# Kernel optimization log

Hardware: AMD Instinct MI355X
Metric: run time of the kernel (lower is better)

Reference implementation:

```python
import jax, jax.numpy as jnp
import numpy as np
from jax import lax

T, B, INP, HS, OUT = 256, 128, 1024, 1024, 1024


def setup_inputs() -> dict:
    key = jax.random.key(0)
    ks = jax.random.split(key, 7)
    s = 1.0 / np.sqrt(HS)  # scale params to keep tanh out of deep saturation
    return {
        "data": jax.random.normal(ks[0], (T, B, INP), jnp.float32),
        "W_ih": jax.random.normal(ks[1], (INP, HS), jnp.float32) * s,
        "W_hh": jax.random.normal(ks[2], (HS, HS), jnp.float32) * s,
        "b_i": jax.random.normal(ks[3], (HS,), jnp.float32) * s,
        "b_h": jax.random.normal(ks[4], (HS,), jnp.float32) * s,
        "W_out": jax.random.normal(ks[5], (OUT, HS), jnp.float32) * s,
        "b_out": jax.random.normal(ks[6], (OUT,), jnp.float32) * s,
    }


def reference(data, W_ih, W_hh, b_i, b_h, W_out, b_out):
    # Elman RNN: h_{t+1} = tanh(x_t @ W_ih + b_i + h_t @ W_hh + b_h)
    bias = b_i + b_h
    h0 = jnp.zeros((data.shape[1], W_hh.shape[0]), data.dtype)

    def step(h, x_t):
        h_new = jnp.tanh(x_t @ W_ih + h @ W_hh + bias)
        return h_new, None

    h_final, _ = lax.scan(step, h0, data)
    # nn.Linear: out = h @ W_out.T + b_out
    return h_final @ W_out.T + b_out
```

## Files before the change

kernel.cpp:

```cpp
#include <hip/hip_runtime.h>
#include <hip/hip_bf16.h>
#include <math.h>


typedef __attribute__((ext_vector_type(8))) short bf16x8;
typedef __attribute__((ext_vector_type(4))) float f32x4;
typedef __attribute__((ext_vector_type(4))) unsigned short u16x4;
typedef __attribute__((ext_vector_type(4))) unsigned int u32x4;
typedef __attribute__((ext_vector_type(2))) unsigned int u32x2;

#define TT 256
#define BB 128
#define HS 1024
#define H_ELEMS (BB * HS)

__device__ __forceinline__ short f2bf(float x) {
  __hip_bfloat16 b = __float2bfloat16(x);
  return *reinterpret_cast<short*>(&b);
}
__device__ __forceinline__ float bf2f(unsigned short s) {
  unsigned int u = ((unsigned int)s) << 16;
  float f;
  __builtin_memcpy(&f, &u, 4);
  return f;
}
__device__ __forceinline__ float fast_exp2(float x) {
#if __has_builtin(__builtin_amdgcn_exp2f)
  return __builtin_amdgcn_exp2f(x);
#else
  return exp2f(x);
#endif
}
__device__ __forceinline__ float fast_rcp(float x) {
#if __has_builtin(__builtin_amdgcn_rcpf)
  return __builtin_amdgcn_rcpf(x);
#else
  return 1.0f / x;
#endif
}
__device__ __forceinline__ float fast_tanh(float x) {
  float xc = fminf(fmaxf(x, -9.0f), 9.0f);
  float e = fast_exp2(2.8853900817779268f * xc);
  return (e - 1.0f) * fast_rcp(e + 1.0f);
}

__device__ __forceinline__ void mall_load_b128(u32x4* dst, const void* p) {
  asm volatile("global_load_dwordx4 %0, %1, off sc0 sc1" : "=v"(*dst) : "v"(p) : "memory");
}
__device__ __forceinline__ void mall_store_b64(void* p, u32x2 v) {
  asm volatile("global_store_dwordx2 %0, %1, off sc0 sc1" :: "v"(p), "v"(v) : "memory");
}
__device__ __forceinline__ void mall_store_b32(void* p, unsigned v) {
  asm volatile("global_store_dword %0, %1, off sc0 sc1" :: "v"(p), "v"(v) : "memory");
}
__device__ __forceinline__ unsigned mall_poll_b32(const void* p) {
  unsigned v;
  asm volatile("global_load_dword %0, %1, off sc0 sc1" : "=v"(v) : "v"(p) : "memory");
  asm volatile("s_waitcnt vmcnt(0)" : "+v"(v));
  return v;
}
__device__ __forceinline__ void wait_vm0() {
  asm volatile("s_waitcnt vmcnt(0)" ::: "memory");
}
#define TIE16(d)                                                        \
  asm volatile("s_waitcnt vmcnt(0)"                                     \
               : "+v"(d[0]), "+v"(d[1]), "+v"(d[2]), "+v"(d[3]),        \
                 "+v"(d[4]), "+v"(d[5]), "+v"(d[6]), "+v"(d[7]),        \
                 "+v"(d[8]), "+v"(d[9]), "+v"(d[10]), "+v"(d[11]),      \
                 "+v"(d[12]), "+v"(d[13]), "+v"(d[14]), "+v"(d[15]))

__global__ __launch_bounds__(256) void cvt_data(const float* __restrict__ src,
                                                __hip_bfloat16* __restrict__ dst) {
  size_t i = ((size_t)blockIdx.x * 256 + threadIdx.x) * 8;
  f32x4 a = *reinterpret_cast<const f32x4*>(src + i);
  f32x4 b = *reinterpret_cast<const f32x4*>(src + i + 4);
  bf16x8 v;
  v[0] = f2bf(a[0]); v[1] = f2bf(a[1]); v[2] = f2bf(a[2]); v[3] = f2bf(a[3]);
  v[4] = f2bf(b[0]); v[5] = f2bf(b[1]); v[6] = f2bf(b[2]); v[7] = f2bf(b[3]);
  *reinterpret_cast<bf16x8*>(dst + i) = v;
}

__global__ __launch_bounds__(256) void cvt_tr(const float* __restrict__ src,
                                              __hip_bfloat16* __restrict__ dst) {
  __shared__ __hip_bfloat16 T[64][72];
  const int tid = threadIdx.x;
  const int k0 = blockIdx.y * 64, n0 = blockIdx.x * 64;
  const int r = tid >> 4, c4 = (tid & 15) * 4;
#pragma unroll
  for (int p = 0; p < 4; ++p) {
    int kk = r + p * 16;
    f32x4 v = *reinterpret_cast<const f32x4*>(src + (size_t)(k0 + kk) * 1024 + n0 + c4);
#pragma unroll
    for (int j = 0; j < 4; ++j) T[c4 + j][kk] = __float2bfloat16(v[j]);
  }
  __syncthreads();
  const int rr = tid >> 3, u = tid & 7;
#pragma unroll
  for (int p = 0; p < 2; ++p) {
    int R = rr + p * 32;
    *reinterpret_cast<bf16x8*>(dst + (size_t)(n0 + R) * 1024 + k0 + u * 8) =
        *reinterpret_cast<const bf16x8*>(&T[R][u * 8]);
  }
}

template <bool ABF>
__global__ __launch_bounds__(256) void gemm_xw2(
    const void* __restrict__ Ain,
    const __hip_bfloat16* __restrict__ Bt,
    const float* __restrict__ b_i,
    const float* __restrict__ b_h,
    __hip_bfloat16* __restrict__ P) {
  __shared__ __hip_bfloat16 As[128][72];
  __shared__ __hip_bfloat16 Bs[128][72];

  const int tid = threadIdx.x;
  const int m0 = blockIdx.y * 128, n0 = blockIdx.x * 128;
  const int wave = tid >> 6, lane = tid & 63;
  const int wm = wave & 1, wn = wave >> 1;
  const int quad = lane >> 4, l16 = lane & 15;
  const int sr = tid >> 3, su = tid & 7;

  f32x4 acc[4][4] = {};

  for (int k0 = 0; k0 < 1024; k0 += 64) {
    __syncthreads();
#pragma unroll
    for (int p = 0; p < 4; ++p) {
      int row = sr + p * 32;
      bf16x8 av;
      if (ABF) {
        av = *reinterpret_cast<const bf16x8*>(
            (const __hip_bfloat16*)Ain + (size_t)(m0 + row) * 1024 + k0 + su * 8);
      } else {
        const float* ap = (const float*)Ain + (size_t)(m0 + row) * 1024 + k0 + su * 8;
        f32x4 x = *reinterpret_cast<const f32x4*>(ap);
        f32x4 y = *reinterpret_cast<const f32x4*>(ap + 4);
        av[0] = f2bf(x[0]); av[1] = f2bf(x[1]); av[2] = f2bf(x[2]); av[3] = f2bf(x[3]);
        av[4] = f2bf(y[0]); av[5] = f2bf(y[1]); av[6] = f2bf(y[2]); av[7] = f2bf(y[3]);
      }
      *reinterpret_cast<bf16x8*>(&As[row][su * 8]) = av;
      bf16x8 bv = *reinterpret_cast<const bf16x8*>(
          Bt + (size_t)(n0 + row) * 1024 + k0 + su * 8);
      *reinterpret_cast<bf16x8*>(&Bs[row][su * 8]) = bv;
    }
    __syncthreads();
#pragma unroll
    for (int kk = 0; kk < 2; ++kk) {
      bf16x8 af[4], bfr[4];
#pragma unroll
      for (int mi = 0; mi < 4; ++mi)
        af[mi] = *reinterpret_cast<const bf16x8*>(&As[wm * 64 + mi * 16 + l16][kk * 32 + quad * 8]);
#pragma unroll
      for (int ni = 0; ni < 4; ++ni)
        bfr[ni] = *reinterpret_cast<const bf16x8*>(&Bs[wn * 64 + ni * 16 + l16][kk * 32 + quad * 8]);
#pragma unroll
      for (int mi = 0; mi < 4; ++mi)
#pragma unroll
        for (int ni = 0; ni < 4; ++ni)
          acc[mi][ni] = __builtin_amdgcn_mfma_f32_16x16x32_bf16(af[mi], bfr[ni], acc[mi][ni], 0, 0, 0);
    }
  }

  float bias[4];
#pragma unroll
  for (int ni = 0; ni < 4; ++ni) {
    int col = n0 + wn * 64 + ni * 16 + l16;
    bias[ni] = b_i[col] + b_h[col];
  }
#pragma unroll
  for (int mi = 0; mi < 4; ++mi)
#pragma unroll
    for (int ni = 0; ni < 4; ++ni) {
      int row = m0 + wm * 64 + mi * 16 + quad * 4;
      int col = n0 + wn * 64 + ni * 16 + l16;
#pragma unroll
      for (int r = 0; r < 4; ++r)
        P[(size_t)(row + r) * 1024 + col] = __float2bfloat16(acc[mi][ni][r] + bias[ni]);
    }
}

__global__ __launch_bounds__(128) void rnn_scan5(
    const __hip_bfloat16* __restrict__ P,
    const float* __restrict__ W_hh,
    __hip_bfloat16* __restrict__ hbuf,
    unsigned* __restrict__ flags) {
  __shared__ __hip_bfloat16 Wt[32 * 1024];
  __shared__ __hip_bfloat16 Ht[16 * 1024];
  __shared__ __hip_bfloat16 Cs[16 * 36];

  const int tid = threadIdx.x;
  const int m = blockIdx.x & 7;
  const int ng = blockIdx.x >> 3;
  const int m0 = m * 16, n0 = ng * 32;

  for (int i = tid; i < 32 * 1024 / 4; i += 128) {
    int nq = i & 7, k = i >> 3;
    f32x4 v = *reinterpret_cast<const f32x4*>(W_hh + (size_t)k * 1024 + n0 + nq * 4);
#pragma unroll
    for (int j = 0; j < 4; ++j) {
      int nl = nq * 4 + j;
      int sg = (k >> 3) ^ (nl & 7);
      Wt[nl * 1024 + sg * 8 + (k & 7)] = __float2bfloat16(v[j]);
    }
  }
  __syncthreads();

  const int r8 = tid >> 3, s8 = tid & 7;
  const int w = tid >> 6, lane = tid & 63;
  const int quad = lane >> 4, l16 = lane & 15;
  const int nl = w * 16 + l16;
  const int col = n0 + nl;
  const int xorl = l16 & 7;
  const int crow = tid >> 3, cseg = tid & 7;
  unsigned* gflags = flags + m * 32;

  for (int t = 0; t < TT; ++t) {
    const __hip_bfloat16* hc = hbuf + (size_t)(t & 1) * H_ELEMS;
    __hip_bfloat16* hn = hbuf + (size_t)((t + 1) & 1) * H_ELEMS;

    const __hip_bfloat16* Pt =
        P + (size_t)t * H_ELEMS + (size_t)(m0 + quad * 4) * 1024 + col;
    unsigned short pv[4];
#pragma unroll
    for (int r = 0; r < 4; ++r)
      pv[r] = *reinterpret_cast<const unsigned short*>(Pt + (size_t)r * 1024);

    if (t > 0) {
      if (tid < 32) {
        const unsigned* fp = gflags + tid;
        int g = 0;
        while (mall_poll_b32(fp) < (unsigned)t && ++g < (1 << 18)) {}
      }
      __syncthreads();
    }

    {
      const char* src = (const char*)(hc + (size_t)(m0 + r8) * 1024) + s8 * 16;
      u32x4 d[16];
#pragma unroll
      for (int i = 0; i < 16; ++i) mall_load_b128(&d[i], src + i * 128);
      TIE16(d);
#pragma unroll
      for (int i = 0; i < 16; ++i) {
        int u = s8 + i * 8;
        int gp = u ^ (r8 & 7) ^ (u >> 4);
        *reinterpret_cast<u32x4*>(&Ht[r8 * 1024 + gp * 8]) = d[i];
      }
    }
    __syncthreads();

    f32x4 acc[4] = {{0.f, 0.f, 0.f, 0.f}, {0.f, 0.f, 0.f, 0.f},
                    {0.f, 0.f, 0.f, 0.f}, {0.f, 0.f, 0.f, 0.f}};
#pragma unroll
    for (int c = 0; c < 8; ++c) {
#pragma unroll
      for (int j = 0; j < 4; ++j) {
        int G = c * 16 + j * 4 + quad;
        int gp = G ^ xorl ^ c;
        bf16x8 af = *reinterpret_cast<const bf16x8*>(&Ht[l16 * 1024 + gp * 8]);
        int sg = G ^ (nl & 7);
        bf16x8 bfrag = *reinterpret_cast<const bf16x8*>(&Wt[nl * 1024 + sg * 8]);
        acc[j] = __builtin_amdgcn_mfma_f32_16x16x32_bf16(af, bfrag, acc[j], 0, 0, 0);
      }
    }

#pragma unroll
    for (int r = 0; r < 4; ++r) {
      float s = (acc[0][r] + acc[1][r]) + (acc[2][r] + acc[3][r]) + bf2f(pv[r]);
      Cs[(quad * 4 + r) * 36 + nl] = __float2bfloat16(fast_tanh(s));
    }
    __syncthreads();
    {
      u32x2 val = *reinterpret_cast<const u32x2*>(&Cs[crow * 36 + cseg * 4]);
      mall_store_b64(hn + (size_t)(m0 + crow) * 1024 + n0 + cseg * 4, val);
      wait_vm0();
    }
    __syncthreads();

    if (t != TT - 1 && tid == 0)
      mall_store_b32(gflags + ng, (unsigned)(t + 1));
  }
}

__global__ __launch_bounds__(256) void gemm_out(
    const __hip_bfloat16* __restrict__ h,
    const float* __restrict__ W_out,
    const float* __restrict__ b_out,
    float* __restrict__ out) {
  const int tid = threadIdx.x;
  const int wave = tid >> 6, lane = tid & 63;
  const int quad = lane >> 4, l16 = lane & 15;
  const int o = blockIdx.x * 64 + wave * 16 + l16;

  f32x4 acc[8] = {};
  for (int k0 = 0; k0 < 1024; k0 += 32) {
    f32x4 w0 = *reinterpret_cast<const f32x4*>(W_out + (size_t)o * 1024 + k0 + quad * 8);
    f32x4 w1 = *reinterpret_cast<const f32x4*>(W_out + (size_t)o * 1024 + k0 + quad * 8 + 4);
    bf16x8 bfr;
    bfr[0] = f2bf(w0[0]); bfr[1] = f2bf(w0[1]); bfr[2] = f2bf(w0[2]); bfr[3] = f2bf(w0[3]);
    bfr[4] = f2bf(w1[0]); bfr[5] = f2bf(w1[1]); bfr[6] = f2bf(w1[2]); bfr[7] = f2bf(w1[3]);
#pragma unroll
    for (int mi = 0; mi < 8; ++mi) {
      bf16x8 af = *reinterpret_cast<const bf16x8*>(h + (size_t)(mi * 16 + l16) * 1024 + k0 + quad * 8);
      acc[mi] = __builtin_amdgcn_mfma_f32_16x16x32_bf16(af, bfr, acc[mi], 0, 0, 0);
    }
  }
  const float bias = b_out[o];
#pragma unroll
  for (int mi = 0; mi < 8; ++mi)
#pragma unroll
    for (int r = 0; r < 4; ++r)
      out[(size_t)(mi * 16 + quad * 4 + r) * 1024 + o] = acc[mi][r] + bias;
}

extern "C" void kernel_launch(void* const* d_in, const int* in_sizes, int n_in,
                              void* d_out, int out_size, void* d_ws, size_t ws_size,
                              hipStream_t stream) {
  const float* data  = (const float*)d_in[0];
  const float* W_ih  = (const float*)d_in[1];
  const float* W_hh  = (const float*)d_in[2];
  const float* b_i   = (const float*)d_in[3];
  const float* b_h   = (const float*)d_in[4];
  const float* W_out = (const float*)d_in[5];
  const float* b_out = (const float*)d_in[6];
  float* out = (float*)d_out;

  char* ws = (char*)d_ws;
  const size_t OFF_P   = 0;
  const size_t OFF_H   = (size_t)TT * H_ELEMS * 2;
  const size_t OFF_FLG = OFF_H + 2 * H_ELEMS * 2;
  const size_t OFF_WT  = OFF_FLG + 1024;
  const size_t OFF_DB  = OFF_WT + 2u * 1024 * 1024;
  const size_t NEED_DB = OFF_DB + (size_t)TT * H_ELEMS * 2;

  __hip_bfloat16* P     = (__hip_bfloat16*)(ws + OFF_P);
  __hip_bfloat16* hbuf  = (__hip_bfloat16*)(ws + OFF_H);
  unsigned* flags       = (unsigned*)(ws + OFF_FLG);
  __hip_bfloat16* W_ihT = (__hip_bfloat16*)(ws + OFF_WT);
  __hip_bfloat16* dataB = (__hip_bfloat16*)(ws + OFF_DB);

  hipMemsetAsync(ws + OFF_H, 0, 2 * H_ELEMS * 2 + 1024, stream);

  cvt_tr<<<dim3(16, 16), 256, 0, stream>>>(W_ih, W_ihT);
  if (ws_size >= NEED_DB) {
    cvt_data<<<16384, 256, 0, stream>>>(data, dataB);
    gemm_xw2<true><<<dim3(8, 256), 256, 0, stream>>>(dataB, W_ihT, b_i, b_h, P);
  } else {
    gemm_xw2<false><<<dim3(8, 256), 256, 0, stream>>>(data, W_ihT, b_i, b_h, P);
  }
  rnn_scan5<<<256, 128, 0, stream>>>(P, W_hh, hbuf, flags);
  gemm_out<<<16, 256, 0, stream>>>(hbuf, W_out, b_out, out);
}
```

Before: 1.129 ms.

## Fuse input projection GEMM into recurrent scan kernel with per-timestep readiness counters

Merges the input-projection GEMM and the recurrent scan into one launch. The first 256 blocks run the scan and the extra 4096 blocks compute P tiles, each bumping a per-timestep counter, so the scan can start while later projection tiles are still being produced. The separate bf16 conversion pass over the input data is dropped in favour of converting inside the GEMM. The scan now loads h fragments straight from global memory into registers with staged waits instead of staging them through shared memory. The scan blocks spin on the counters, which relies on them being co-resident with the GEMM blocks and adds polling traffic.

Measured after the change: 1.429 ms. 1.27x slower.

```diff
diff --git a/kernel.cpp b/kernel.cpp
--- a/kernel.cpp
+++ b/kernel.cpp
@@ -5,7 +5,6 @@
 
 typedef __attribute__((ext_vector_type(8))) short bf16x8;
 typedef __attribute__((ext_vector_type(4))) float f32x4;
-typedef __attribute__((ext_vector_type(4))) unsigned short u16x4;
 typedef __attribute__((ext_vector_type(4))) unsigned int u32x4;
 typedef __attribute__((ext_vector_type(2))) unsigned int u32x2;
 
@@ -13,6 +12,7 @@
 #define BB 128
 #define HS 1024
 #define H_ELEMS (BB * HS)
+#define SMEM_BYTES 66688
 
 __device__ __forceinline__ short f2bf(float x) {
   __hip_bfloat16 b = __float2bfloat16(x);
@@ -44,8 +44,14 @@
   return (e - 1.0f) * fast_rcp(e + 1.0f);
 }
 
-__device__ __forceinline__ void mall_load_b128(u32x4* dst, const void* p) {
+__device__ __forceinline__ void mall_load_bf8(bf16x8* dst, const void* p) {
   asm volatile("global_load_dwordx4 %0, %1, off sc0 sc1" : "=v"(*dst) : "v"(p) : "memory");
+}
+__device__ __forceinline__ void mall_load_u16(unsigned* dst, const void* p) {
+  asm volatile("global_load_ushort %0, %1, off sc0 sc1" : "=v"(*dst) : "v"(p) : "memory");
+}
+__device__ __forceinline__ void mall_store_b128(void* p, u32x4 v) {
+  asm volatile("global_store_dwordx4 %0, %1, off sc0 sc1" :: "v"(p), "v"(v) : "memory");
 }
 __device__ __forceinline__ void mall_store_b64(void* p, u32x2 v) {
   asm volatile("global_store_dwordx2 %0, %1, off sc0 sc1" :: "v"(p), "v"(v) : "memory");
@@ -62,22 +68,14 @@
 __device__ __forceinline__ void wait_vm0() {
   asm volatile("s_waitcnt vmcnt(0)" ::: "memory");
 }
-#define TIE16(d)                                                        \
-  asm volatile("s_waitcnt vmcnt(0)"                                     \
-               : "+v"(d[0]), "+v"(d[1]), "+v"(d[2]), "+v"(d[3]),        \
-                 "+v"(d[4]), "+v"(d[5]), "+v"(d[6]), "+v"(d[7]),        \
-                 "+v"(d[8]), "+v"(d[9]), "+v"(d[10]), "+v"(d[11]),      \
-                 "+v"(d[12]), "+v"(d[13]), "+v"(d[14]), "+v"(d[15]))
-
-__global__ __launch_bounds__(256) void cvt_data(const float* __restrict__ src,
-                                                __hip_bfloat16* __restrict__ dst) {
-  size_t i = ((size_t)blockIdx.x * 256 + threadIdx.x) * 8;
-  f32x4 a = *reinterpret_cast<const f32x4*>(src + i);
-  f32x4 b = *reinterpret_cast<const f32x4*>(src + i + 4);
-  bf16x8 v;
-  v[0] = f2bf(a[0]); v[1] = f2bf(a[1]); v[2] = f2bf(a[2]); v[3] = f2bf(a[3]);
-  v[4] = f2bf(b[0]); v[5] = f2bf(b[1]); v[6] = f2bf(b[2]); v[7] = f2bf(b[3]);
-  *reinterpret_cast<bf16x8*>(dst + i) = v;
+#define WAITV(N) asm volatile("s_waitcnt vmcnt(" #N ")" ::: "memory")
+__device__ __forceinline__ void tie8(bf16x8& a, bf16x8& b, bf16x8& c, bf16x8& d,
+                                     bf16x8& e, bf16x8& f, bf16x8& g, bf16x8& h) {
+  asm volatile("" : "+v"(a), "+v"(b), "+v"(c), "+v"(d),
+                    "+v"(e), "+v"(f), "+v"(g), "+v"(h));
+}
+__device__ __forceinline__ void tie4u(unsigned& a, unsigned& b, unsigned& c, unsigned& d) {
+  asm volatile("" : "+v"(a), "+v"(b), "+v"(c), "+v"(d));
 }
 
 __global__ __launch_bounds__(256) void cvt_tr(const float* __restrict__ src,
@@ -103,92 +101,99 @@
   }
 }
 
-template <bool ABF>
-__global__ __launch_bounds__(256) void gemm_xw2(
-    const void* __restrict__ Ain,
-    const __hip_bfloat16* __restrict__ Bt,
+__global__ __launch_bounds__(128) void fused(
+    const float* __restrict__ data,
+    const __hip_bfloat16* __restrict__ W_ihT,
+    const float* __restrict__ W_hh,
     const float* __restrict__ b_i,
     const float* __restrict__ b_h,
-    __hip_bfloat16* __restrict__ P) {
-  __shared__ __hip_bfloat16 As[128][72];
-  __shared__ __hip_bfloat16 Bs[128][72];
-
+    __hip_bfloat16* __restrict__ P,
+    __hip_bfloat16* __restrict__ hbuf,
+    unsigned* __restrict__ flags,
+    unsigned* __restrict__ pcnt) {
+  __shared__ __attribute__((aligned(16))) unsigned char smem[SMEM_BYTES];
   const int tid = threadIdx.x;
-  const int m0 = blockIdx.y * 128, n0 = blockIdx.x * 128;
-  const int wave = tid >> 6, lane = tid & 63;
-  const int wm = wave & 1, wn = wave >> 1;
+  const int w = tid >> 6, lane = tid & 63;
   const int quad = lane >> 4, l16 = lane & 15;
-  const int sr = tid >> 3, su = tid & 7;
-
-  f32x4 acc[4][4] = {};
-
-  for (int k0 = 0; k0 < 1024; k0 += 64) {
-    __syncthreads();
-#pragma unroll
-    for (int p = 0; p < 4; ++p) {
-      int row = sr + p * 32;
-      bf16x8 av;
-      if (ABF) {
-        av = *reinterpret_cast<const bf16x8*>(
-            (const __hip_bfloat16*)Ain + (size_t)(m0 + row) * 1024 + k0 + su * 8);
-      } else {
-        const float* ap = (const float*)Ain + (size_t)(m0 + row) * 1024 + k0 + su * 8;
+
+  if (blockIdx.x >= 256) {
+    auto As = (__hip_bfloat16(*)[72])(smem);
+    auto Bs = (__hip_bfloat16(*)[72])(smem + 18432);
+    const int j = (int)blockIdx.x - 256;
+    const int mt = j >> 4, nt = j & 15;
+    const int m0g = mt * 128, n0g = nt * 64;
+    const int sr = tid >> 3, su = tid & 7;
+
+    float bias[4];
+#pragma unroll
+    for (int ni = 0; ni < 4; ++ni) {
+      int c = n0g + ni * 16 + l16;
+      bias[ni] = b_i[c] + b_h[c];
+    }
+
+    f32x4 acc[4][4] = {};
+    for (int k0 = 0; k0 < 1024; k0 += 64) {
+      __syncthreads();
+#pragma unroll
+      for (int p = 0; p < 8; ++p) {
+        int row = sr + p * 16;
+        const float* ap = data + (size_t)(m0g + row) * 1024 + k0 + su * 8;
         f32x4 x = *reinterpret_cast<const f32x4*>(ap);
         f32x4 y = *reinterpret_cast<const f32x4*>(ap + 4);
+        bf16x8 av;
         av[0] = f2bf(x[0]); av[1] = f2bf(x[1]); av[2] = f2bf(x[2]); av[3] = f2bf(x[3]);
         av[4] = f2bf(y[0]); av[5] = f2bf(y[1]); av[6] = f2bf(y[2]); av[7] = f2bf(y[3]);
-      }
-      *reinterpret_cast<bf16x8*>(&As[row][su * 8]) = av;
-      bf16x8 bv = *reinterpret_cast<const bf16x8*>(
-          Bt + (size_t)(n0 + row) * 1024 + k0 + su * 8);
-      *reinterpret_cast<bf16x8*>(&Bs[row][su * 8]) = bv;
-    }
-    __syncthreads();
-#pragma unroll
-    for (int kk = 0; kk < 2; ++kk) {
-      bf16x8 af[4], bfr[4];
-#pragma unroll
-      for (int mi = 0; mi < 4; ++mi)
-        af[mi] = *reinterpret_cast<const bf16x8*>(&As[wm * 64 + mi * 16 + l16][kk * 32 + quad * 8]);
+        *reinterpret_cast<bf16x8*>(&As[row][su * 8]) = av;
+      }
+#pragma unroll
+      for (int p = 0; p < 4; ++p) {
+        int n = sr + p * 16;
+        *reinterpret_cast<bf16x8*>(&Bs[n][su * 8]) = *reinterpret_cast<const bf16x8*>(
+            W_ihT + (size_t)(n0g + n) * 1024 + k0 + su * 8);
+      }
+      __syncthreads();
+#pragma unroll
+      for (int kk = 0; kk < 2; ++kk) {
+        bf16x8 af[4], bfr[4];
+#pragma unroll
+        for (int mi = 0; mi < 4; ++mi)
+          af[mi] = *reinterpret_cast<const bf16x8*>(&As[w * 64 + mi * 16 + l16][kk * 32 + quad * 8]);
+#pragma unroll
+        for (int ni = 0; ni < 4; ++ni)
+          bfr[ni] = *reinterpret_cast<const bf16x8*>(&Bs[ni * 16 + l16][kk * 32 + quad * 8]);
+#pragma unroll
+        for (int mi = 0; mi < 4; ++mi)
+#pragma unroll
+          for (int ni = 0; ni < 4; ++ni)
+            acc[mi][ni] = __builtin_amdgcn_mfma_f32_16x16x32_bf16(af[mi], bfr[ni], acc[mi][ni], 0, 0, 0);
+      }
+    }
+    __syncthreads();
+#pragma unroll
+    for (int mi = 0; mi < 4; ++mi)
 #pragma unroll
       for (int ni = 0; ni < 4; ++ni)
-        bfr[ni] = *reinterpret_cast<const bf16x8*>(&Bs[wn * 64 + ni * 16 + l16][kk * 32 + quad * 8]);
-#pragma unroll
-      for (int mi = 0; mi < 4; ++mi)
-#pragma unroll
-        for (int ni = 0; ni < 4; ++ni)
-          acc[mi][ni] = __builtin_amdgcn_mfma_f32_16x16x32_bf16(af[mi], bfr[ni], acc[mi][ni], 0, 0, 0);
-    }
-  }
-
-  float bias[4];
-#pragma unroll
-  for (int ni = 0; ni < 4; ++ni) {
-    int col = n0 + wn * 64 + ni * 16 + l16;
-    bias[ni] = b_i[col] + b_h[col];
-  }
-#pragma unroll
-  for (int mi = 0; mi < 4; ++mi)
-#pragma unroll
-    for (int ni = 0; ni < 4; ++ni) {
-      int row = m0 + wm * 64 + mi * 16 + quad * 4;
-      int col = n0 + wn * 64 + ni * 16 + l16;
-#pragma unroll
-      for (int r = 0; r < 4; ++r)
-        P[(size_t)(row + r) * 1024 + col] = __float2bfloat16(acc[mi][ni][r] + bias[ni]);
-    }
-}
-
-__global__ __launch_bounds__(128) void rnn_scan5(
-    const __hip_bfloat16* __restrict__ P,
-    const float* __restrict__ W_hh,
-    __hip_bfloat16* __restrict__ hbuf,
-    unsigned* __restrict__ flags) {
-  __shared__ __hip_bfloat16 Wt[32 * 1024];
-  __shared__ __hip_bfloat16 Ht[16 * 1024];
-  __shared__ __hip_bfloat16 Cs[16 * 36];
-
-  const int tid = threadIdx.x;
+#pragma unroll
+        for (int r = 0; r < 4; ++r)
+          As[w * 64 + mi * 16 + quad * 4 + r][ni * 16 + l16] =
+              __float2bfloat16(acc[mi][ni][r] + bias[ni]);
+    __syncthreads();
+    {
+      __hip_bfloat16* Prow = P + (size_t)(m0g + tid) * 1024 + n0g;
+#pragma unroll
+      for (int s = 0; s < 8; ++s) {
+        u32x4 v = *reinterpret_cast<const u32x4*>(&As[tid][s * 8]);
+        mall_store_b128(Prow + s * 8, v);
+      }
+      wait_vm0();
+    }
+    __syncthreads();
+    if (tid == 0) atomicAdd(pcnt + mt, 1u);
+    return;
+  }
+
+  __hip_bfloat16* Wt = (__hip_bfloat16*)smem;
+  __hip_bfloat16* Cs = (__hip_bfloat16*)(smem + 65536);
   const int m = blockIdx.x & 7;
   const int ng = blockIdx.x >> 3;
   const int m0 = m * 16, n0 = ng * 32;
@@ -197,20 +202,16 @@
     int nq = i & 7, k = i >> 3;
     f32x4 v = *reinterpret_cast<const f32x4*>(W_hh + (size_t)k * 1024 + n0 + nq * 4);
 #pragma unroll
-    for (int j = 0; j < 4; ++j) {
-      int nl = nq * 4 + j;
-      int sg = (k >> 3) ^ (nl & 7);
-      Wt[nl * 1024 + sg * 8 + (k & 7)] = __float2bfloat16(v[j]);
+    for (int jj = 0; jj < 4; ++jj) {
+      int nl2 = nq * 4 + jj;
+      int sg = (k >> 3) ^ (nl2 & 7);
+      Wt[nl2 * 1024 + sg * 8 + (k & 7)] = __float2bfloat16(v[jj]);
     }
   }
   __syncthreads();
 
-  const int r8 = tid >> 3, s8 = tid & 7;
-  const int w = tid >> 6, lane = tid & 63;
-  const int quad = lane >> 4, l16 = lane & 15;
   const int nl = w * 16 + l16;
   const int col = n0 + nl;
-  const int xorl = l16 & 7;
   const int crow = tid >> 3, cseg = tid & 7;
   unsigned* gflags = flags + m * 32;
 
@@ -218,55 +219,60 @@
     const __hip_bfloat16* hc = hbuf + (size_t)(t & 1) * H_ELEMS;
     __hip_bfloat16* hn = hbuf + (size_t)((t + 1) & 1) * H_ELEMS;
 
+    if (tid < 33) {
+      const unsigned* fp = (tid < 32) ? (gflags + tid) : (pcnt + t);
+      unsigned tgt = (tid < 32) ? (unsigned)t : 16u;
+      int g = 0;
+      while (mall_poll_b32(fp) < tgt && ++g < (1 << 20)) {}
+    }
+    __syncthreads();
+
     const __hip_bfloat16* Pt =
         P + (size_t)t * H_ELEMS + (size_t)(m0 + quad * 4) * 1024 + col;
-    unsigned short pv[4];
-#pragma unroll
-    for (int r = 0; r < 4; ++r)
-      pv[r] = *reinterpret_cast<const unsigned short*>(Pt + (size_t)r * 1024);
-
-    if (t > 0) {
-      if (tid < 32) {
-        const unsigned* fp = gflags + tid;
-        int g = 0;
-        while (mall_poll_b32(fp) < (unsigned)t && ++g < (1 << 18)) {}
-      }
-      __syncthreads();
-    }
-
-    {
-      const char* src = (const char*)(hc + (size_t)(m0 + r8) * 1024) + s8 * 16;
-      u32x4 d[16];
-#pragma unroll
-      for (int i = 0; i < 16; ++i) mall_load_b128(&d[i], src + i * 128);
-      TIE16(d);
-#pragma unroll
-      for (int i = 0; i < 16; ++i) {
-        int u = s8 + i * 8;
-        int gp = u ^ (r8 & 7) ^ (u >> 4);
-        *reinterpret_cast<u32x4*>(&Ht[r8 * 1024 + gp * 8]) = d[i];
-      }
-    }
-    __syncthreads();
+    unsigned pv0, pv1, pv2, pv3;
+    mall_load_u16(&pv0, Pt);
+    mall_load_u16(&pv1, Pt + 1024);
+    mall_load_u16(&pv2, Pt + 2048);
+    mall_load_u16(&pv3, Pt + 3072);
+    const __hip_bfloat16* hrow = hc + (size_t)(m0 + l16) * 1024 + quad * 8;
+    bf16x8 fr[8][4];
+#pragma unroll
+    for (int c = 0; c < 8; ++c)
+#pragma unroll
+      for (int jj = 0; jj < 4; ++jj)
+        mall_load_bf8(&fr[c][jj], hrow + c * 128 + jj * 32);
 
     f32x4 acc[4] = {{0.f, 0.f, 0.f, 0.f}, {0.f, 0.f, 0.f, 0.f},
                     {0.f, 0.f, 0.f, 0.f}, {0.f, 0.f, 0.f, 0.f}};
 #pragma unroll
-    for (int c = 0; c < 8; ++c) {
-#pragma unroll
-      for (int j = 0; j < 4; ++j) {
-        int G = c * 16 + j * 4 + quad;
-        int gp = G ^ xorl ^ c;
-        bf16x8 af = *reinterpret_cast<const bf16x8*>(&Ht[l16 * 1024 + gp * 8]);
-        int sg = G ^ (nl & 7);
-        bf16x8 bfrag = *reinterpret_cast<const bf16x8*>(&Wt[nl * 1024 + sg * 8]);
-        acc[j] = __builtin_amdgcn_mfma_f32_16x16x32_bf16(af, bfrag, acc[j], 0, 0, 0);
-      }
-    }
-
+    for (int cc = 0; cc < 4; ++cc) {
+      if (cc == 0) { WAITV(24); tie8(fr[0][0], fr[0][1], fr[0][2], fr[0][3],
+                                     fr[1][0], fr[1][1], fr[1][2], fr[1][3]); }
+      else if (cc == 1) { WAITV(16); tie8(fr[2][0], fr[2][1], fr[2][2], fr[2][3],
+                                          fr[3][0], fr[3][1], fr[3][2], fr[3][3]); }
+      else if (cc == 2) { WAITV(8); tie8(fr[4][0], fr[4][1], fr[4][2], fr[4][3],
+                                         fr[5][0], fr[5][1], fr[5][2], fr[5][3]); }
+      else { WAITV(0); tie8(fr[6][0], fr[6][1], fr[6][2], fr[6][3],
+                            fr[7][0], fr[7][1], fr[7][2], fr[7][3]);
+             tie4u(pv0, pv1, pv2, pv3); }
+#pragma unroll
+      for (int h2 = 0; h2 < 2; ++h2) {
+        int c = cc * 2 + h2;
+#pragma unroll
+        for (int jj = 0; jj < 4; ++jj) {
+          int G = c * 16 + jj * 4 + quad;
+          int sg = G ^ (nl & 7);
+          bf16x8 bfrag = *reinterpret_cast<const bf16x8*>(&Wt[nl * 1024 + sg * 8]);
+          acc[jj] = __builtin_amdgcn_mfma_f32_16x16x32_bf16(fr[c][jj], bfrag, acc[jj], 0, 0, 0);
+        }
+      }
+    }
+
+    unsigned pvv[4] = {pv0, pv1, pv2, pv3};
 #pragma unroll
     for (int r = 0; r < 4; ++r) {
-      float s = (acc[0][r] + acc[1][r]) + (acc[2][r] + acc[3][r]) + bf2f(pv[r]);
+      float s = (acc[0][r] + acc[1][r]) + (acc[2][r] + acc[3][r]) +
+                bf2f((unsigned short)pvv[r]);
       Cs[(quad * 4 + r) * 36 + nl] = __float2bfloat16(fast_tanh(s));
     }
     __syncthreads();
@@ -329,25 +335,19 @@
   const size_t OFF_P   = 0;
   const size_t OFF_H   = (size_t)TT * H_ELEMS * 2;
   const size_t OFF_FLG = OFF_H + 2 * H_ELEMS * 2;
-  const size_t OFF_WT  = OFF_FLG + 1024;
-  const size_t OFF_DB  = OFF_WT + 2u * 1024 * 1024;
-  const size_t NEED_DB = OFF_DB + (size_t)TT * H_ELEMS * 2;
+  const size_t OFF_PC  = OFF_FLG + 1024;
+  const size_t OFF_WT  = OFF_PC + 1024;
 
   __hip_bfloat16* P     = (__hip_bfloat16*)(ws + OFF_P);
   __hip_bfloat16* hbuf  = (__hip_bfloat16*)(ws + OFF_H);
   unsigned* flags       = (unsigned*)(ws + OFF_FLG);
+  unsigned* pcnt        = (unsigned*)(ws + OFF_PC);
   __hip_bfloat16* W_ihT = (__hip_bfloat16*)(ws + OFF_WT);
-  __hip_bfloat16* dataB = (__hip_bfloat16*)(ws + OFF_DB);
-
-  hipMemsetAsync(ws + OFF_H, 0, 2 * H_ELEMS * 2 + 1024, stream);
+
+  hipMemsetAsync(ws + OFF_H, 0, 2 * H_ELEMS * 2 + 2048, stream);
 
   cvt_tr<<<dim3(16, 16), 256, 0, stream>>>(W_ih, W_ihT);
-  if (ws_size >= NEED_DB) {
-    cvt_data<<<16384, 256, 0, stream>>>(data, dataB);
-    gemm_xw2<true><<<dim3(8, 256), 256, 0, stream>>>(dataB, W_ihT, b_i, b_h, P);
-  } else {
-    gemm_xw2<false><<<dim3(8, 256), 256, 0, stream>>>(data, W_ihT, b_i, b_h, P);
-  }
-  rnn_scan5<<<256, 128, 0, stream>>>(P, W_hh, hbuf, flags);
+  fused<<<256 + 4096, 128, 0, stream>>>(data, W_ihT, W_hh, b_i, b_h,
+                                        P, hbuf, flags, pcnt);
   gemm_out<<<16, 256, 0, stream>>>(hbuf, W_out, b_out, out);
 }
```
